# Performance work log

Hardware: AMD Instinct MI355X
Metric: run time of the kernel (lower is better)

Reference implementation:

```python
import jax, jax.numpy as jnp
import numpy as np

# dims
N, E, B, T = 1024, 8192, 4, 8          # nodes, edges, batch, time steps
IN, HID, H, NCLASS = 64, 64, 4, 7      # in_dim, nhidden, heads, nclass
K = N - NCLASS + 1                     # output-head conv width
NEG, EPS = 0.2, 1e-5


def setup_inputs() -> dict:
    key = jax.random.key(0)
    ks = jax.random.split(key, 24)
    p = lambda i, shape: jax.random.normal(ks[i], shape, jnp.float32) * 0.05
    inputs = jax.random.normal(ks[0], (B, IN, T, N), jnp.float32)
    src = jax.random.randint(ks[1], (E,), 0, N, jnp.int32)
    dst = jnp.repeat(jnp.arange(N, dtype=jnp.int32), E // N)  # every node has in-degree 8
    return {
        "inputs": inputs, "src": src, "dst": dst,
        "W0": p(2, (H * HID, IN)), "al0": p(3, (H, HID)), "ar0": p(4, (H, HID)),
        "W1": p(5, (H * HID, H * HID)), "al1": p(6, (H, HID)), "ar1": p(7, (H, HID)),
        "W2": p(8, (H * 1, H * HID)), "al2": p(9, (H, 1)), "ar2": p(10, (H, 1)),
        "Wres2": p(11, (H * 1, H * HID)),
        # Outputlayer
        "tc1_w": p(12, (H, H, T)), "tc1_b": p(13, (H,)),
        "ln1_g": jnp.ones((N, H), jnp.float32), "ln1_b": jnp.zeros((N, H), jnp.float32),
        "tc2_w": p(14, (1, H)), "tc2_b": p(15, (1,)),
        "ln2_g": jnp.ones((N, 1), jnp.float32), "ln2_b": jnp.zeros((N, 1), jnp.float32),
        "fc_w": p(16, (K,)), "fc_b": p(17, (1,)),
    }


def _gat_conv(h, src, dst, W, al, ar, res=None, act=None):
    # h: (N,B,T,F) -> feat: (N,B,T,H,D)
    heads, d = al.shape
    feat = (h @ W.T).reshape(N, B, T, heads, d)
    el = jnp.einsum('nbthd,hd->nbth', feat, al)
    er = jnp.einsum('nbthd,hd->nbth', feat, ar)
    e = jax.nn.leaky_relu(el[src] + er[dst], NEG)           # (E,B,T,H)
    emax = jax.ops.segment_max(e, dst, num_segments=N)
    ex = jnp.exp(e - emax[dst])
    den = jax.ops.segment_sum(ex, dst, num_segments=N)
    a = ex / den[dst]                                        # edge softmax over incoming edges
    out = jax.ops.segment_sum(feat[src] * a[..., None], dst, num_segments=N)  # (N,B,T,H,D)
    if res is not None:
        out = out + res
    if act is not None:
        out = act(out)
    return out


def reference(inputs, src, dst,
              W0, al0, ar0, W1, al1, ar1, W2, al2, ar2, Wres2,
              tc1_w, tc1_b, ln1_g, ln1_b, tc2_w, tc2_b, ln2_g, ln2_b, fc_w, fc_b):
    # (B,IN,T,N) -> (N,B,T,IN) : transpose(0,3).transpose(1,3)
    h = jnp.transpose(inputs.astype(jnp.float32), (3, 0, 2, 1))
    h1 = _gat_conv(h, src, dst, W0, al0, ar0, act=jax.nn.elu).reshape(N, B, T, H * HID)
    h2 = _gat_conv(h1, src, dst, W1, al1, ar1,
                   res=h1.reshape(N, B, T, H, HID), act=jax.nn.elu).reshape(N, B, T, H * HID)
    res2 = (h2 @ Wres2.T).reshape(N, B, T, H, 1)
    o = _gat_conv(h2, src, dst, W2, al2, ar2, res=res2)      # (N,B,T,H,1)
    # transpose(1,3).transpose(0,3).squeeze(-1) -> (B,H,T,N)
    x = jnp.transpose(o[..., 0], (1, 3, 2, 0))

    # Outputlayer
    # tconv1: Conv2d(H->H, kernel (T,1)) collapses time -> (B,H,N)
    x1 = jnp.einsum('oht,bhtn->bon', tc1_w, x) + tc1_b[None, :, None]
    # ln1: LayerNorm over (N,H) of (B,1,N,H)
    z = jnp.transpose(x1, (0, 2, 1))                          # (B,N,H)
    mu = z.mean(axis=(1, 2), keepdims=True)
    var = z.var(axis=(1, 2), keepdims=True)
    z = (z - mu) / jnp.sqrt(var + EPS) * ln1_g + ln1_b
    x1 = jnp.transpose(z, (0, 2, 1))                          # (B,H,N)
    # tconv2: 1x1 conv H->1 -> (B,1,N)
    x2 = jnp.einsum('oh,bhn->bon', tc2_w, x1) + tc2_b[None, :, None]
    # ln2: LayerNorm over (N,1)
    mu = x2.mean(axis=2, keepdims=True)
    var = x2.var(axis=2, keepdims=True)
    x2 = (x2 - mu) / jnp.sqrt(var + EPS) * ln2_g[:, 0] + ln2_b[:, 0]
    # fc: Conv2d(1->1, kernel (1,K)) sliding over nodes -> (B,NCLASS)
    xc = x2[:, :, None, :]                                    # (B,1,1,N) NCHW
    w = fc_w[None, None, None, :]                             # (1,1,1,K) OIHW
    out = jax.lax.conv_general_dilated(xc, w, (1, 1), 'VALID') + fc_b[None, :, None, None]
    return out[:, 0, 0, :]                                    # (B, NCLASS)
```

## Files before the change

### kernel.cpp

```cpp
#include <hip/hip_runtime.h>
#include <math.h>

#define NEGS 0.2f
#define EPSF 1e-5f

typedef short s16x8 __attribute__((ext_vector_type(8)));
typedef float f32x4 __attribute__((ext_vector_type(4)));

__device__ __forceinline__ float b2f(unsigned short u) {
  union { unsigned int i; float f; } v; v.i = ((unsigned int)u) << 16; return v.f;
}
__device__ __forceinline__ unsigned short f2b(float f) {
  union { float f; unsigned int i; } v; v.f = f;
  unsigned int x = v.i;
  return (unsigned short)((x + 0x7fffu + ((x >> 16) & 1u)) >> 16);
}

__device__ __forceinline__ void gbar(int* slot, int nb) {
  __syncthreads();
  if (threadIdx.x == 0) {
    int* cnt  = slot;
    int* flag = slot + 32;
    int old = __hip_atomic_fetch_add(cnt, 1, __ATOMIC_RELAXED, __HIP_MEMORY_SCOPE_AGENT);
    if (old == nb - 1) {
      __hip_atomic_store(flag, 1, __ATOMIC_RELEASE, __HIP_MEMORY_SCOPE_AGENT);
    } else {
      int it = 0;
      while (__hip_atomic_load(flag, __ATOMIC_RELAXED, __HIP_MEMORY_SCOPE_AGENT) == 0) {
        __builtin_amdgcn_s_sleep(2);
        if (++it > (1 << 22)) break;
      }
    }
  }
  __syncthreads();
}

__global__ __launch_bounds__(256, 4) void k_mega(
    const float* __restrict__ inp, const int* __restrict__ src,
    const float* __restrict__ W0, const float* __restrict__ al0, const float* __restrict__ ar0,
    const float* __restrict__ W1, const float* __restrict__ al1, const float* __restrict__ ar1,
    const float* __restrict__ W2, const float* __restrict__ al2, const float* __restrict__ ar2,
    const float* __restrict__ Wr2,
    unsigned short* __restrict__ W1bX, unsigned short* __restrict__ feat0,
    unsigned short* __restrict__ feat1,
    float* __restrict__ el0, float* __restrict__ er0,
    float* __restrict__ el1, float* __restrict__ er1,
    float* __restrict__ feat2, float* __restrict__ res2,
    float* __restrict__ o2, int* bar)
{
  __shared__ __align__(16) char pool[22528];
  const int tid = threadIdx.x;
  const int bid = blockIdx.x;
  const int g     = bid & 7;
  const int bt    = g*4 + ((bid >> 3) & 3);
  const int nBase = (bid >> 5) * 32;
  const int b = bt >> 3, t = bt & 7;
  const int w = tid >> 6, lane = tid & 63, n16 = lane & 15, q = lane >> 4;

  s16x8 h1r[2][2];

  {
    unsigned short (*At)[72] = (unsigned short(*)[72])pool;
    unsigned short *Lb = (unsigned short*)(pool + 4608);
    s16x8 bf[2][4];
    #pragma unroll
    for (int kc = 0; kc < 2; ++kc)
      #pragma unroll
      for (int ct = 0; ct < 4; ++ct) {
        const float* p = &W0[(size_t)((w*4 + ct)*16 + n16)*64 + kc*32 + q*8];
        float4 wa = *(const float4*)p;
        float4 wb = *(const float4*)(p + 4);
        s16x8 o;
        o[0]=(short)f2b(wa.x); o[1]=(short)f2b(wa.y); o[2]=(short)f2b(wa.z); o[3]=(short)f2b(wa.w);
        o[4]=(short)f2b(wb.x); o[5]=(short)f2b(wb.y); o[6]=(short)f2b(wb.z); o[7]=(short)f2b(wb.w);
        bf[kc][ct] = o;
      }
    {
      const int nn = tid & 31, cg = tid >> 5;
      #pragma unroll
      for (int c2 = 0; c2 < 4; ++c2) {
        const int ch = cg*8 + c2*2;
        float vx = inp[((size_t)(b*64 + ch  )*8 + t)*1024 + nBase + nn];
        float vy = inp[((size_t)(b*64 + ch+1)*8 + t)*1024 + nBase + nn];
        unsigned int pk = ((unsigned int)f2b(vy) << 16) | (unsigned int)f2b(vx);
        *(unsigned int*)&At[nn][ch] = pk;
      }
    }
    __syncthreads();
    f32x4 acc[2][4];
    #pragma unroll
    for (int rt = 0; rt < 2; ++rt)
      #pragma unroll
      for (int ct = 0; ct < 4; ++ct) acc[rt][ct] = (f32x4){0.f,0.f,0.f,0.f};
    #pragma unroll
    for (int kc = 0; kc < 2; ++kc) {
      s16x8 af[2];
      #pragma unroll
      for (int rt = 0; rt < 2; ++rt)
        af[rt] = *(const s16x8*)&At[rt*16 + n16][kc*32 + q*8];
      #pragma unroll
      for (int rt = 0; rt < 2; ++rt)
        #pragma unroll
        for (int ct = 0; ct < 4; ++ct)
          acc[rt][ct] = __builtin_amdgcn_mfma_f32_16x16x32_bf16(af[rt], bf[kc][ct], acc[rt][ct], 0, 0, 0);
    }
    float alv[4], arv[4];
    #pragma unroll
    for (int ct = 0; ct < 4; ++ct) {
      alv[ct] = al0[w*64 + ct*16 + n16];
      arv[ct] = ar0[w*64 + ct*16 + n16];
    }
    #pragma unroll
    for (int rt = 0; rt < 2; ++rt) {
      #pragma unroll
      for (int reg = 0; reg < 4; ++reg) {
        float pl = acc[rt][0][reg]*alv[0] + acc[rt][1][reg]*alv[1]
                 + acc[rt][2][reg]*alv[2] + acc[rt][3][reg]*alv[3];
        float pr = acc[rt][0][reg]*arv[0] + acc[rt][1][reg]*arv[1]
                 + acc[rt][2][reg]*arv[2] + acc[rt][3][reg]*arv[3];
        #pragma unroll
        for (int o = 1; o < 16; o <<= 1) { pl += __shfl_xor(pl, o); pr += __shfl_xor(pr, o); }
        if (n16 == 0) {
          int r = (nBase + rt*16 + q*4 + reg)*32 + bt;
          el0[r*4 + w] = pl;
          er0[r*4 + w] = pr;
        }
      }
    }
    #pragma unroll
    for (int rt = 0; rt < 2; ++rt)
      #pragma unroll
      for (int ct = 0; ct < 4; ++ct)
        #pragma unroll
        for (int reg = 0; reg < 4; ++reg)
          Lb[(rt*16 + q*4 + reg)*256 + w*64 + ct*16 + n16] = f2b(acc[rt][ct][reg]);
    __syncthreads();
    #pragma unroll
    for (int i = 0; i < 4; ++i) {
      int u = tid + i*256;
      int m = u >> 5, off = (u & 31) * 8;
      *(s16x8*)&feat0[(size_t)((nBase + m)*32 + bt)*256 + off] = *(const s16x8*)&Lb[m*256 + off];
    }
    {
      const int j = ((bid >> 3) << 9) + tid*2;
      float2 wv2 = *(const float2*)&W1[j];
      W1bX[(size_t)g*65536 + j]     = f2b(wv2.x);
      W1bX[(size_t)g*65536 + j + 1] = f2b(wv2.y);
    }
  }
  gbar(bar + (0*8 + g)*64, 128);

  {
    float (*wsm)[8][4] = (float(*)[8][4])pool;
    int   (*ssm)[8]    = (int(*)[8])(pool + 4096);
    unsigned short *smbuf = (unsigned short*)(pool + 5120);
    unsigned short (*At)[264] = (unsigned short(*)[264])smbuf;
    unsigned short *Lb = smbuf;
    ((int*)ssm)[tid] = src[nBase*8 + tid];
    __syncthreads();
    if (tid < 128) {
      const int nl = tid >> 2, h = tid & 3;
      const int rn = (nBase + nl)*32 + bt;
      const float erv = er0[rn*4 + h];
      float e[8]; float mx = -1e30f;
      #pragma unroll
      for (int j = 0; j < 8; ++j) {
        float v = el0[(ssm[nl][j]*32 + bt)*4 + h] + erv;
        v = v >= 0.f ? v : NEGS * v;
        e[j] = v; mx = fmaxf(mx, v);
      }
      float den = 0.f;
      #pragma unroll
      for (int j = 0; j < 8; ++j) { e[j] = __expf(e[j] - mx); den += e[j]; }
      const float inv = 1.f / den;
      #pragma unroll
      for (int j = 0; j < 8; ++j) wsm[nl][j][h] = e[j] * inv;
    }
    __syncthreads();
    {
      const int hw2 = tid >> 5, l5 = tid & 31;
      const int c0 = l5 * 8, hh = l5 >> 3;
      #pragma unroll
      for (int p2 = 0; p2 < 2; ++p2) {
        const int nlA = p2*16 + hw2, nlB = nlA + 8;
        s16x8 vA[8], vB[8];
        #pragma unroll
        for (int j = 0; j < 8; ++j) {
          vA[j] = *(const s16x8*)&feat0[(size_t)(ssm[nlA][j]*32 + bt)*256 + c0];
          vB[j] = *(const s16x8*)&feat0[(size_t)(ssm[nlB][j]*32 + bt)*256 + c0];
        }
        asm volatile("" ::: "memory");
        float aA[8] = {0,0,0,0,0,0,0,0}, aB[8] = {0,0,0,0,0,0,0,0};
        #pragma unroll
        for (int j = 0; j < 8; ++j) {
          const float wA = wsm[nlA][j][hh], wB = wsm[nlB][j][hh];
          #pragma unroll
          for (int i = 0; i < 8; ++i) {
            aA[i] = fmaf(wA, b2f((unsigned short)vA[j][i]), aA[i]);
            aB[i] = fmaf(wB, b2f((unsigned short)vB[j][i]), aB[i]);
          }
        }
        s16x8 oA, oB;
        #pragma unroll
        for (int i = 0; i < 8; ++i) {
          float xA = aA[i] > 0.f ? aA[i] : expm1f(aA[i]);
          float xB = aB[i] > 0.f ? aB[i] : expm1f(aB[i]);
          oA[i] = (short)f2b(xA); oB[i] = (short)f2b(xB);
        }
        *(s16x8*)&At[nlA][c0] = oA;
        *(s16x8*)&At[nlB][c0] = oB;
        h1r[p2][0] = oA;
        h1r[p2][1] = oB;
      }
    }
    __syncthreads();
    f32x4 acc[2][4];
    #pragma unroll
    for (int rt = 0; rt < 2; ++rt)
      #pragma unroll
      for (int ct = 0; ct < 4; ++ct) acc[rt][ct] = (f32x4){0.f,0.f,0.f,0.f};
    const unsigned short* W1g = W1bX + (size_t)g*65536;
    #pragma unroll
    for (int kc = 0; kc < 8; ++kc) {
      s16x8 af[2], bfr[4];
      #pragma unroll
      for (int rt = 0; rt < 2; ++rt)
        af[rt] = *(const s16x8*)&At[rt*16 + n16][kc*32 + q*8];
      #pragma unroll
      for (int ct = 0; ct < 4; ++ct)
        bfr[ct] = *(const s16x8*)&W1g[(size_t)((w*4 + ct)*16 + n16)*256 + kc*32 + q*8];
      #pragma unroll
      for (int rt = 0; rt < 2; ++rt)
        #pragma unroll
        for (int ct = 0; ct < 4; ++ct)
          acc[rt][ct] = __builtin_amdgcn_mfma_f32_16x16x32_bf16(af[rt], bfr[ct], acc[rt][ct], 0, 0, 0);
    }
    float alv[4], arv[4];
    #pragma unroll
    for (int ct = 0; ct < 4; ++ct) {
      alv[ct] = al1[w*64 + ct*16 + n16];
      arv[ct] = ar1[w*64 + ct*16 + n16];
    }
    #pragma unroll
    for (int rt = 0; rt < 2; ++rt) {
      #pragma unroll
      for (int reg = 0; reg < 4; ++reg) {
        float pl = acc[rt][0][reg]*alv[0] + acc[rt][1][reg]*alv[1]
                 + acc[rt][2][reg]*alv[2] + acc[rt][3][reg]*alv[3];
        float pr = acc[rt][0][reg]*arv[0] + acc[rt][1][reg]*arv[1]
                 + acc[rt][2][reg]*arv[2] + acc[rt][3][reg]*arv[3];
        #pragma unroll
        for (int o = 1; o < 16; o <<= 1) { pl += __shfl_xor(pl, o); pr += __shfl_xor(pr, o); }
        if (n16 == 0) {
          int r = (nBase + rt*16 + q*4 + reg)*32 + bt;
          el1[r*4 + w] = pl;
          er1[r*4 + w] = pr;
        }
      }
    }
    __syncthreads();
    #pragma unroll
    for (int rt = 0; rt < 2; ++rt)
      #pragma unroll
      for (int ct = 0; ct < 4; ++ct)
        #pragma unroll
        for (int reg = 0; reg < 4; ++reg)
          Lb[(rt*16 + q*4 + reg)*256 + w*64 + ct*16 + n16] = f2b(acc[rt][ct][reg]);
    __syncthreads();
    #pragma unroll
    for (int i = 0; i < 4; ++i) {
      int u = tid + i*256;
      int row = u >> 5, off = (u & 31) * 8;
      *(s16x8*)&feat1[(size_t)((nBase + row)*32 + bt)*256 + off] = *(const s16x8*)&Lb[row*256 + off];
    }
  }
  gbar(bar + (1*8 + g)*64, 128);

  {
    float (*wsm)[8][4] = (float(*)[8][4])pool;
    int   (*ssm)[8]    = (int(*)[8])(pool + 4096);
    float (*Wp)[256]   = (float(*)[256])(pool + 5120);
    ((int*)ssm)[tid] = src[nBase*8 + tid];
    for (int j2 = tid; j2 < 2048; j2 += 256) {
      int o = j2 >> 8, k = j2 & 255;
      Wp[o][k] = (o < 4) ? W2[o*256 + k] : Wr2[(o-4)*256 + k];
    }
    __syncthreads();
    if (tid < 128) {
      const int nl = tid >> 2, h = tid & 3;
      const int rn = (nBase + nl)*32 + bt;
      const float erv = er1[rn*4 + h];
      float e[8]; float mx = -1e30f;
      #pragma unroll
      for (int j = 0; j < 8; ++j) {
        float v = el1[(ssm[nl][j]*32 + bt)*4 + h] + erv;
        v = v >= 0.f ? v : NEGS * v;
        e[j] = v; mx = fmaxf(mx, v);
      }
      float den = 0.f;
      #pragma unroll
      for (int j = 0; j < 8; ++j) { e[j] = __expf(e[j] - mx); den += e[j]; }
      const float inv = 1.f / den;
      #pragma unroll
      for (int j = 0; j < 8; ++j) wsm[nl][j][h] = e[j] * inv;
    }
    __syncthreads();
    const int hw2 = tid >> 5, l5 = tid & 31;
    const int c0 = l5 * 8, hh = l5 >> 3;
    #pragma unroll
    for (int p2 = 0; p2 < 2; ++p2) {
      const int nlA = p2*16 + hw2, nlB = nlA + 8;
      const int rnA = (nBase + nlA)*32 + bt, rnB = (nBase + nlB)*32 + bt;
      s16x8 vA[8], vB[8];
      const s16x8 rrA = h1r[p2][0], rrB = h1r[p2][1];
      #pragma unroll
      for (int j = 0; j < 8; ++j) {
        vA[j] = *(const s16x8*)&feat1[(size_t)(ssm[nlA][j]*32 + bt)*256 + c0];
        vB[j] = *(const s16x8*)&feat1[(size_t)(ssm[nlB][j]*32 + bt)*256 + c0];
      }
      asm volatile("" ::: "memory");
      float aA[8] = {0,0,0,0,0,0,0,0}, aB[8] = {0,0,0,0,0,0,0,0};
      #pragma unroll
      for (int j = 0; j < 8; ++j) {
        const float wA = wsm[nlA][j][hh], wB = wsm[nlB][j][hh];
        #pragma unroll
        for (int i = 0; i < 8; ++i) {
          aA[i] = fmaf(wA, b2f((unsigned short)vA[j][i]), aA[i]);
          aB[i] = fmaf(wB, b2f((unsigned short)vB[j][i]), aB[i]);
        }
      }
      #pragma unroll
      for (int i = 0; i < 8; ++i) {
        float xA = aA[i] + b2f((unsigned short)rrA[i]);
        float xB = aB[i] + b2f((unsigned short)rrB[i]);
        aA[i] = xA > 0.f ? xA : expm1f(xA);
        aB[i] = xB > 0.f ? xB : expm1f(xB);
      }
      #pragma unroll
      for (int o = 0; o < 8; ++o) {
        float4 wa = *(const float4*)&Wp[o][c0];
        float4 wb = *(const float4*)&Wp[o][c0 + 4];
        float pA = aA[0]*wa.x + aA[1]*wa.y + aA[2]*wa.z + aA[3]*wa.w
                 + aA[4]*wb.x + aA[5]*wb.y + aA[6]*wb.z + aA[7]*wb.w;
        float pB = aB[0]*wa.x + aB[1]*wa.y + aB[2]*wa.z + aB[3]*wa.w
                 + aB[4]*wb.x + aB[5]*wb.y + aB[6]*wb.z + aB[7]*wb.w;
        #pragma unroll
        for (int off = 1; off < 32; off <<= 1) {
          pA += __shfl_xor(pA, off);
          pB += __shfl_xor(pB, off);
        }
        if (l5 == 0) {
          if (o < 4) { feat2[rnA*4 + o] = pA; feat2[rnB*4 + o] = pB; }
          else       { res2[rnA*4 + (o-4)] = pA; res2[rnB*4 + (o-4)] = pB; }
        }
      }
    }
  }
  gbar(bar + (2*8 + g)*64, 128);

  if (tid < 128) {
    const int nl = tid >> 2, h = tid & 3;
    const int n = nBase + nl;
    const int rn = n*32 + bt;
    const float av = al2[h], rv = ar2[h];
    const float erv = feat2[rn*4 + h] * rv;
    float f[8], e[8]; float m = -1e30f;
    #pragma unroll
    for (int j = 0; j < 8; ++j) {
      const int s_ = src[n*8 + j];
      f[j] = feat2[(s_*32 + bt)*4 + h];
      float v = f[j]*av + erv;
      v = v >= 0.f ? v : NEGS * v;
      e[j] = v; m = fmaxf(m, v);
    }
    float den = 0.f, num = 0.f;
    #pragma unroll
    for (int j = 0; j < 8; ++j) { float ex = __expf(e[j]-m); den += ex; num = fmaf(ex, f[j], num); }
    o2[rn*4 + h] = num/den + res2[rn*4 + h];
  }
}

__global__ __launch_bounds__(256) void k_fin(
    const float* __restrict__ o2, const float* __restrict__ tc1w, const float* __restrict__ tc1b,
    const float* __restrict__ ln1g, const float* __restrict__ ln1b,
    const float* __restrict__ tc2w, const float* __restrict__ tc2b,
    const float* __restrict__ ln2g, const float* __restrict__ ln2b,
    const float* __restrict__ fcw, const float* __restrict__ fcb,
    float* __restrict__ out)
{
  __shared__ __align__(16) float x1s[4][1024];
  __shared__ float x2s[1024];
  __shared__ float tc1s[128];
  __shared__ float redA[4], redB[4];
  __shared__ float redC[4][7];
  const int bb = blockIdx.x, tid = threadIdx.x;
  const int wv = tid >> 6, lane = tid & 63;
  if (tid < 128) tc1s[tid] = tc1w[tid];
  __syncthreads();
  float s = 0.f, qq = 0.f;
  #pragma unroll
  for (int i = 0; i < 4; ++i) {
    const int n = tid + i*256;
    const float4* p = (const float4*)&o2[(size_t)(n*32 + bb*8)*4];
    float vv[8][4];
    #pragma unroll
    for (int tt = 0; tt < 8; ++tt) {
      float4 f4 = p[tt];
      vv[tt][0]=f4.x; vv[tt][1]=f4.y; vv[tt][2]=f4.z; vv[tt][3]=f4.w;
    }
    #pragma unroll
    for (int o = 0; o < 4; ++o) {
      float a = tc1b[o];
      #pragma unroll
      for (int h = 0; h < 4; ++h)
        #pragma unroll
        for (int tt = 0; tt < 8; ++tt)
          a = fmaf(tc1s[(o*4+h)*8 + tt], vv[tt][h], a);
      x1s[o][n] = a; s += a; qq += a*a;
    }
  }
  #pragma unroll
  for (int o = 32; o > 0; o >>= 1) { s += __shfl_down(s, o); qq += __shfl_down(qq, o); }
  if (lane == 0) { redA[wv] = s; redB[wv] = qq; }
  __syncthreads();
  const float S = redA[0]+redA[1]+redA[2]+redA[3];
  const float Q = redB[0]+redB[1]+redB[2]+redB[3];
  const float mu  = S * (1.f/4096.f);
  const float var = Q * (1.f/4096.f) - mu*mu;
  const float inv = rsqrtf(var + EPSF);
  const float tb = tc2b[0];
  const float r0 = tc2w[0], r1 = tc2w[1], r2 = tc2w[2], r3 = tc2w[3];
  float accv[4]; float s2 = 0.f, q2 = 0.f;
  #pragma unroll
  for (int i = 0; i < 4; ++i) {
    const int n = tid + i*256;
    float4 g4 = *(const float4*)&ln1g[n*4];
    float4 b4 = *(const float4*)&ln1b[n*4];
    float a = tb;
    a = fmaf(r0, (x1s[0][n]-mu)*inv*g4.x + b4.x, a);
    a = fmaf(r1, (x1s[1][n]-mu)*inv*g4.y + b4.y, a);
    a = fmaf(r2, (x1s[2][n]-mu)*inv*g4.z + b4.z, a);
    a = fmaf(r3, (x1s[3][n]-mu)*inv*g4.w + b4.w, a);
    accv[i] = a; s2 += a; q2 += a*a;
  }
  __syncthreads();
  #pragma unroll
  for (int o = 32; o > 0; o >>= 1) { s2 += __shfl_down(s2, o); q2 += __shfl_down(q2, o); }
  if (lane == 0) { redA[wv] = s2; redB[wv] = q2; }
  __syncthreads();
  const float S2 = redA[0]+redA[1]+redA[2]+redA[3];
  const float Q2 = redB[0]+redB[1]+redB[2]+redB[3];
  const float mu2  = S2 * (1.f/1024.f);
  const float inv2 = rsqrtf(Q2 * (1.f/1024.f) - mu2*mu2 + EPSF);
  #pragma unroll
  for (int i = 0; i < 4; ++i) {
    const int n = tid + i*256;
    x2s[n] = (accv[i] - mu2) * inv2 * ln2g[n] + ln2b[n];
  }
  __syncthreads();
  float pc[7] = {0.f,0.f,0.f,0.f,0.f,0.f,0.f};
  for (int k = tid; k < 1018; k += 256) {
    const float fw = fcw[k];
    #pragma unroll
    for (int c = 0; c < 7; ++c) pc[c] = fmaf(x2s[k + c], fw, pc[c]);
  }
  #pragma unroll
  for (int o = 32; o > 0; o >>= 1)
    #pragma unroll
    for (int c = 0; c < 7; ++c) pc[c] += __shfl_down(pc[c], o);
  if (lane == 0) {
    #pragma unroll
    for (int c = 0; c < 7; ++c) redC[wv][c] = pc[c];
  }
  __syncthreads();
  if (tid < 7)
    out[bb*7 + tid] = redC[0][tid] + redC[1][tid] + redC[2][tid] + redC[3][tid] + fcb[0];
}

extern "C" void kernel_launch(void* const* d_in, const int* in_sizes, int n_in,
                              void* d_out, int out_size, void* d_ws, size_t ws_size,
                              hipStream_t stream)
{
  const float* inp  = (const float*)d_in[0];
  const int*   src  = (const int*)  d_in[1];
  const float* W0   = (const float*)d_in[3];
  const float* al0  = (const float*)d_in[4];
  const float* ar0  = (const float*)d_in[5];
  const float* W1   = (const float*)d_in[6];
  const float* al1  = (const float*)d_in[7];
  const float* ar1  = (const float*)d_in[8];
  const float* W2   = (const float*)d_in[9];
  const float* al2  = (const float*)d_in[10];
  const float* ar2  = (const float*)d_in[11];
  const float* Wr2  = (const float*)d_in[12];
  const float* tc1w = (const float*)d_in[13];
  const float* tc1b = (const float*)d_in[14];
  const float* ln1g = (const float*)d_in[15];
  const float* ln1b = (const float*)d_in[16];
  const float* tc2w = (const float*)d_in[17];
  const float* tc2b = (const float*)d_in[18];
  const float* ln2g = (const float*)d_in[19];
  const float* ln2b = (const float*)d_in[20];
  const float* fcw  = (const float*)d_in[21];
  const float* fcb  = (const float*)d_in[22];
  float* out = (float*)d_out;

  unsigned short* W1bX   = (unsigned short*)d_ws;
  unsigned short* featb0 = W1bX   + 524288;
  unsigned short* featb1 = featb0 + 8388608;
  float* el0   = (float*)(featb1 + 8388608);
  float* er0   = el0   + 131072;
  float* el1   = er0   + 131072;
  float* er1   = el1   + 131072;
  float* feat2 = er1   + 131072;
  float* res2  = feat2 + 131072;
  float* o2b   = res2  + 131072;
  int*   bar   = (int*)(o2b + 131072);

  hipMemsetAsync(bar, 0, 6144, stream);
  k_mega<<<dim3(1024), dim3(256), 0, stream>>>(inp, src, W0, al0, ar0, W1, al1, ar1,
                                               W2, al2, ar2, Wr2,
                                               W1bX, featb0, featb1,
                                               el0, er0, el1, er1, feat2, res2, o2b, bar);
  k_fin<<<dim3(4), dim3(256), 0, stream>>>(o2b, tc1w, tc1b, ln1g, ln1b, tc2w, tc2b,
                                           ln2g, ln2b, fcw, fcb, out);
}
```

Measured before the change: 181.1 us.

## Fuse temporal conv into final GAT stage via atomics and use fast exp for ELU

The tconv1 time-collapse is moved from the final kernel into the last GAT layer's epilogue. Each thread reduces its head contribution across a 4-lane shuffle and atomically adds into a small (B,H,N) buffer that is zeroed together with the barrier counters. This shrinks the final kernel's reads from the full per-time-step output to the reduced buffer. ELU's expm1f is replaced with __expf(x)-1, which is cheaper but loses precision near zero, and the layer-2 source indices are read from shared memory instead of global. The atomic accumulation makes summation order nondeterministic, and the shared-memory index array is assumed to still hold valid data at that point.

```diff
diff --git a/kernel.cpp b/kernel.cpp
--- a/kernel.cpp
+++ b/kernel.cpp
@@ -15,6 +15,7 @@
   unsigned int x = v.i;
   return (unsigned short)((x + 0x7fffu + ((x >> 16) & 1u)) >> 16);
 }
+__device__ __forceinline__ float elu_neg(float x) { return __expf(x) - 1.f; }
 
 __device__ __forceinline__ void gbar(int* slot, int nb) {
   __syncthreads();
@@ -40,13 +41,13 @@
     const float* __restrict__ W0, const float* __restrict__ al0, const float* __restrict__ ar0,
     const float* __restrict__ W1, const float* __restrict__ al1, const float* __restrict__ ar1,
     const float* __restrict__ W2, const float* __restrict__ al2, const float* __restrict__ ar2,
-    const float* __restrict__ Wr2,
+    const float* __restrict__ Wr2, const float* __restrict__ tc1w,
     unsigned short* __restrict__ W1bX, unsigned short* __restrict__ feat0,
     unsigned short* __restrict__ feat1,
     float* __restrict__ el0, float* __restrict__ er0,
     float* __restrict__ el1, float* __restrict__ er1,
     float* __restrict__ feat2, float* __restrict__ res2,
-    float* __restrict__ o2, int* bar)
+    float* __restrict__ x1, int* bar)
 {
   __shared__ __align__(16) char pool[22528];
   const int tid = threadIdx.x;
@@ -203,8 +204,8 @@
         s16x8 oA, oB;
         #pragma unroll
         for (int i = 0; i < 8; ++i) {
-          float xA = aA[i] > 0.f ? aA[i] : expm1f(aA[i]);
-          float xB = aB[i] > 0.f ? aB[i] : expm1f(aB[i]);
+          float xA = aA[i] > 0.f ? aA[i] : elu_neg(aA[i]);
+          float xB = aB[i] > 0.f ? aB[i] : elu_neg(aB[i]);
           oA[i] = (short)f2b(xA); oB[i] = (short)f2b(xB);
         }
         *(s16x8*)&At[nlA][c0] = oA;
@@ -333,8 +334,8 @@
       for (int i = 0; i < 8; ++i) {
         float xA = aA[i] + b2f((unsigned short)rrA[i]);
         float xB = aB[i] + b2f((unsigned short)rrB[i]);
-        aA[i] = xA > 0.f ? xA : expm1f(xA);
-        aB[i] = xB > 0.f ? xB : expm1f(xB);
+        aA[i] = xA > 0.f ? xA : elu_neg(xA);
+        aB[i] = xB > 0.f ? xB : elu_neg(xB);
       }
       #pragma unroll
       for (int o = 0; o < 8; ++o) {
@@ -358,30 +359,41 @@
   }
   gbar(bar + (2*8 + g)*64, 128);
 
-  if (tid < 128) {
-    const int nl = tid >> 2, h = tid & 3;
-    const int n = nBase + nl;
-    const int rn = n*32 + bt;
-    const float av = al2[h], rv = ar2[h];
-    const float erv = feat2[rn*4 + h] * rv;
-    float f[8], e[8]; float m = -1e30f;
-    #pragma unroll
-    for (int j = 0; j < 8; ++j) {
-      const int s_ = src[n*8 + j];
-      f[j] = feat2[(s_*32 + bt)*4 + h];
-      float v = f[j]*av + erv;
-      v = v >= 0.f ? v : NEGS * v;
-      e[j] = v; m = fmaxf(m, v);
-    }
-    float den = 0.f, num = 0.f;
-    #pragma unroll
-    for (int j = 0; j < 8; ++j) { float ex = __expf(e[j]-m); den += ex; num = fmaf(ex, f[j], num); }
-    o2[rn*4 + h] = num/den + res2[rn*4 + h];
+  {
+    int (*ssm)[8] = (int(*)[8])(pool + 4096);
+    if (tid < 128) {
+      const int nl = tid >> 2, h = tid & 3;
+      const int n = nBase + nl;
+      const int rn = n*32 + bt;
+      const float av = al2[h], rv = ar2[h];
+      const float erv = feat2[rn*4 + h] * rv;
+      float f[8], e[8]; float m = -1e30f;
+      #pragma unroll
+      for (int j = 0; j < 8; ++j) {
+        f[j] = feat2[(ssm[nl][j]*32 + bt)*4 + h];
+        float v = f[j]*av + erv;
+        v = v >= 0.f ? v : NEGS * v;
+        e[j] = v; m = fmaxf(m, v);
+      }
+      float den = 0.f, num = 0.f;
+      #pragma unroll
+      for (int j = 0; j < 8; ++j) { float ex = __expf(e[j]-m); den += ex; num = fmaf(ex, f[j], num); }
+      const float os = num/den + res2[rn*4 + h];
+      float po[4];
+      #pragma unroll
+      for (int o = 0; o < 4; ++o) po[o] = tc1w[(o*4 + h)*8 + t] * os;
+      #pragma unroll
+      for (int off = 1; off < 4; off <<= 1)
+        #pragma unroll
+        for (int o = 0; o < 4; ++o) po[o] += __shfl_xor(po[o], off);
+      float v = (h==0) ? po[0] : (h==1) ? po[1] : (h==2) ? po[2] : po[3];
+      atomicAdd(&x1[(b*4 + h)*1024 + n], v);
+    }
   }
 }
 
 __global__ __launch_bounds__(256) void k_fin(
-    const float* __restrict__ o2, const float* __restrict__ tc1w, const float* __restrict__ tc1b,
+    const float* __restrict__ x1g, const float* __restrict__ tc1b,
     const float* __restrict__ ln1g, const float* __restrict__ ln1b,
     const float* __restrict__ tc2w, const float* __restrict__ tc2b,
     const float* __restrict__ ln2g, const float* __restrict__ ln2b,
@@ -390,32 +402,17 @@
 {
   __shared__ __align__(16) float x1s[4][1024];
   __shared__ float x2s[1024];
-  __shared__ float tc1s[128];
   __shared__ float redA[4], redB[4];
   __shared__ float redC[4][7];
   const int bb = blockIdx.x, tid = threadIdx.x;
   const int wv = tid >> 6, lane = tid & 63;
-  if (tid < 128) tc1s[tid] = tc1w[tid];
-  __syncthreads();
   float s = 0.f, qq = 0.f;
   #pragma unroll
   for (int i = 0; i < 4; ++i) {
     const int n = tid + i*256;
-    const float4* p = (const float4*)&o2[(size_t)(n*32 + bb*8)*4];
-    float vv[8][4];
-    #pragma unroll
-    for (int tt = 0; tt < 8; ++tt) {
-      float4 f4 = p[tt];
-      vv[tt][0]=f4.x; vv[tt][1]=f4.y; vv[tt][2]=f4.z; vv[tt][3]=f4.w;
-    }
     #pragma unroll
     for (int o = 0; o < 4; ++o) {
-      float a = tc1b[o];
-      #pragma unroll
-      for (int h = 0; h < 4; ++h)
-        #pragma unroll
-        for (int tt = 0; tt < 8; ++tt)
-          a = fmaf(tc1s[(o*4+h)*8 + tt], vv[tt][h], a);
+      float a = x1g[(bb*4 + o)*1024 + n] + tc1b[o];
       x1s[o][n] = a; s += a; qq += a*a;
     }
   }
@@ -514,14 +511,14 @@
   float* er1   = el1   + 131072;
   float* feat2 = er1   + 131072;
   float* res2  = feat2 + 131072;
-  float* o2b   = res2  + 131072;
-  int*   bar   = (int*)(o2b + 131072);
-
-  hipMemsetAsync(bar, 0, 6144, stream);
+  float* x1    = res2  + 131072;
+  int*   bar   = (int*)(x1 + 16384);
+
+  hipMemsetAsync(x1, 0, 16384*4 + 6144, stream);
   k_mega<<<dim3(1024), dim3(256), 0, stream>>>(inp, src, W0, al0, ar0, W1, al1, ar1,
-                                               W2, al2, ar2, Wr2,
+                                               W2, al2, ar2, Wr2, tc1w,
                                                W1bX, featb0, featb1,
-                                               el0, er0, el1, er1, feat2, res2, o2b, bar);
-  k_fin<<<dim3(4), dim3(256), 0, stream>>>(o2b, tc1w, tc1b, ln1g, ln1b, tc2w, tc2b,
+                                               el0, er0, el1, er1, feat2, res2, x1, bar);
+  k_fin<<<dim3(4), dim3(256), 0, stream>>>(x1, tc1b, ln1g, ln1b, tc2w, tc2b,
                                            ln2g, ln2b, fcw, fcb, out);
 }
```

Result: faster. 173.2 us (-4.3%).
